# Optimization experiments

Measured on AMD Instinct MI355X. Metric: run time of the kernel, lower is better.

The kernel has to match this reference:

```python
import jax, jax.numpy as jnp
import numpy as np

N_FFT = 64
HOP = 32
PAD = N_FFT // 2

def _window():
    # torch.hann_window(n_fft) is periodic: 0.5*(1 - cos(2*pi*n/N))
    n = jnp.arange(N_FFT, dtype=jnp.float32)
    return 0.5 * (1.0 - jnp.cos(2.0 * jnp.pi * n / N_FFT))

def _frame_idx(n_frames):
    return jnp.arange(n_frames)[:, None] * HOP + jnp.arange(N_FFT)[None, :]

def _stft(x):
    # x: [..., T] -> complex spectrogram [..., n_frames, F] (torch center=True, reflect pad)
    xp = jnp.pad(x, [(0, 0)] * (x.ndim - 1) + [(PAD, PAD)], mode='reflect')
    Tp = xp.shape[-1]
    n_frames = (Tp - N_FFT) // HOP + 1
    frames = xp[..., _frame_idx(n_frames)] * _window()  # [..., n_frames, n_fft]
    return jnp.fft.rfft(frames, axis=-1)

def _istft(spec, T):
    # spec: [..., n_frames, F] -> signal [..., T] (torch istft with length=T)
    w = _window()
    frames = jnp.fft.irfft(spec, n=N_FFT, axis=-1) * w  # [..., n_frames, n_fft]
    n_frames = frames.shape[-2]
    Tp = T + 2 * PAD
    idx = _frame_idx(n_frames)
    ola = jnp.zeros(frames.shape[:-2] + (Tp,), frames.dtype).at[..., idx].add(frames)
    env = jnp.zeros((Tp,), frames.dtype).at[idx].add(w * w)
    env = jnp.where(env > 1e-11, env, 1.0)
    return (ola / env)[..., PAD:PAD + T]

def reference(x, weight):
    # x: [B, C_in, T], weight: [C_out, C_in, F]
    B, C, T = x.shape
    U = _stft(x)  # [B, C_in, n_frames, F] complex
    # Linearity: sum over input channels in frequency domain, then one ISTFT per output channel.
    Yr = jnp.einsum('oif,binf->bonf', weight, U.real)
    Yi = jnp.einsum('oif,binf->bonf', weight, U.imag)
    Y = Yr + 1j * Yi  # [B, C_out, n_frames, F]
    return _istft(Y, T)  # [B, C_out, T]

def setup_inputs() -> dict:
    key = jax.random.key(0)
    k1, k2 = jax.random.split(key)
    B, C_in, C_out, T = 8, 64, 64, 16384
    x = jax.random.normal(k1, (B, C_in, T), dtype=jnp.float32)
    weight = jax.random.normal(k2, (C_out, C_in, N_FFT // 2 + 1), dtype=jnp.float32)
    return {"x": x, "weight": weight}
```

## Files before the change

kernel.cpp:

```cpp
#include <hip/hip_runtime.h>
#include <cstddef>

#define TT 16384
#define NFRAMES 513
#define NFP 520
#define BNP (8 * NFP)
#define PI32 0.09817477042468103870f

typedef unsigned int u32;
typedef unsigned short u16;
typedef __attribute__((ext_vector_type(8))) short bf16x8;
typedef __attribute__((ext_vector_type(4))) float f32x4;

#define TAB_WBF 0
#define TAB_BM  (33 * 64 * 72)
#define TAB_BTA (TAB_BM + 80 * 72)
#define TAB_TOT (TAB_BTA + 64 * 104)
#define TF_EINV 0

__device__ __forceinline__ float b2f(u16 h) {
  union { u32 u; float f; } v; v.u = ((u32)h) << 16; return v.f;
}
__device__ __forceinline__ u16 f2b(float f) {
  union { float f; u32 u; } v; v.f = f;
  const u32 r = v.u + 0x7FFFu + ((v.u >> 16) & 1u);
  return (u16)(r >> 16);
}
__device__ __forceinline__ u32 pack2(float a, float b) {
  return (u32)f2b(a) | ((u32)f2b(b) << 16);
}
__device__ __forceinline__ float2 b2x2(u32 u) {
  union { u32 u; float f; } lo, hi;
  lo.u = u << 16; hi.u = u & 0xFFFF0000u;
  return make_float2(lo.f, hi.f);
}

__global__ __launch_bounds__(256) void k0_tables(const float* __restrict__ W,
                                                 u16* __restrict__ t16,
                                                 float* __restrict__ tf) {
  const int b = blockIdx.x, tid = threadIdx.x;
  if (b < 33) {
    for (int idx = tid; idx < 64 * 72; idx += 256) {
      const int o = idx / 72, i = idx % 72;
      const float v = (i < 64) ? W[(size_t)(o * 64 + i) * 33 + b] : 0.f;
      t16[TAB_WBF + b * 64 * 72 + idx] = f2b(v);
    }
  } else if (b == 33) {
    for (int idx = tid; idx < 80 * 72; idx += 256) {
      const int fc = idx / 72, j = idx % 72;
      float v = 0.f;
      if (j < 64 && fc < 65) {
        const float wj = 0.5f * (1.0f - cosf((float)j * PI32));
        if (fc < 64) {
          const int f = fc >> 1;
          const float ang = (float)((f * j) & 63) * PI32;
          v = wj * ((fc & 1) ? -sinf(ang) : cosf(ang));
        } else {
          v = (j & 1) ? -wj : wj;
        }
      }
      t16[TAB_BM + idx] = f2b(v);
    }
  } else {
    for (int idx = tid; idx < 64 * 104; idx += 256) {
      const int j = idx / 104, cf = idx % 104;
      float v = 0.f;
      if (cf < 66) {
        const int f = cf >> 1;
        const float wj = 0.5f * (1.0f - cosf((float)j * PI32));
        const float sc = ((f == 0) || (f == 32)) ? 0.015625f : 0.03125f;
        const float ang = (float)((f * j) & 63) * PI32;
        v = wj * sc * ((cf & 1) ? -sinf(ang) : cosf(ang));
      }
      t16[TAB_BTA + idx] = f2b(v);
    }
    if (tid < 32) {
      const float c = cosf((float)tid * PI32);
      tf[TF_EINV + tid] = 2.0f / (1.0f + c * c);
    }
  }
}

__global__ __launch_bounds__(256) void k1_stft(const float* __restrict__ x,
                                               const u16* __restrict__ t16,
                                               u16* __restrict__ U) {
  const int tile = blockIdx.x;
  const int ch   = blockIdx.y;
  const int b    = blockIdx.z;
  const int tid = threadIdx.x;
  __shared__ __align__(16) u16 Bm[80 * 72];
  __shared__ __align__(16) u16 Awt[64 * 72];
  __shared__ __align__(16) u16 Cs[66 * 72];
  __shared__ float xef[64];

  for (int k = tid; k < 720; k += 256)
    ((uint4*)Bm)[k] = ((const uint4*)(t16 + TAB_BM))[k];

  const float* xb = x + (size_t)(b * 64 + ch) * TT;

  if (tile == 8) {
    if (tid < 64) {
      const int t = (tid < 32) ? (16352 + tid) : (16414 - tid);
      xef[tid] = xb[t];
    }
    __syncthreads();
    if (tid < 66) {
      float s = 0.f;
#pragma unroll 8
      for (int j = 0; j < 64; ++j)
        s = fmaf(xef[j], b2f(Bm[tid * 72 + j]), s);
      U[(size_t)(tid * 64 + ch) * BNP + b * NFP + 512] = f2b(s);
    }
    return;
  }

  const int F0 = tile * 64;
  if (tile == 0) {
    if (tid < 32) Awt[tid] = f2b(xb[32 - tid]);
    for (int c = 8 + tid; c < 520; c += 256) {
      const float4 v = *(const float4*)(xb + 4 * c - 32);
      const uint2 pk = make_uint2(pack2(v.x, v.y), pack2(v.z, v.w));
      const int flb = c >> 3, jj = 4 * (c & 7);
      if (flb < 64) *(uint2*)&Awt[flb * 72 + jj] = pk;
      *(uint2*)&Awt[(flb - 1) * 72 + 32 + jj] = pk;
    }
  } else {
    const float* src = xb + 32 * F0 - 32;
    for (int c = tid; c < 520; c += 256) {
      const float4 v = *(const float4*)(src + 4 * c);
      const uint2 pk = make_uint2(pack2(v.x, v.y), pack2(v.z, v.w));
      const int flb = c >> 3, jj = 4 * (c & 7);
      if (flb < 64) *(uint2*)&Awt[flb * 72 + jj] = pk;
      if (flb >= 1) *(uint2*)&Awt[(flb - 1) * 72 + 32 + jj] = pk;
    }
  }
  __syncthreads();

  const int wave = tid >> 6, lane = tid & 63;
  const int n = lane & 15, quad = lane >> 4;

  bf16x8 bfr[4][2];
#pragma unroll
  for (int nt = 0; nt < 4; ++nt)
#pragma unroll
    for (int ks = 0; ks < 2; ++ks)
      bfr[nt][ks] = *(const bf16x8*)&Awt[(nt * 16 + n) * 72 + ks * 32 + quad * 8];

  const int npass = (wave == 0) ? 2 : 1;
  for (int pass = 0; pass < npass; ++pass) {
    const int mt = pass ? 4 : wave;
    bf16x8 af[2];
#pragma unroll
    for (int ks = 0; ks < 2; ++ks)
      af[ks] = *(const bf16x8*)&Bm[(mt * 16 + n) * 72 + ks * 32 + quad * 8];
    f32x4 acc[4];
#pragma unroll
    for (int nt = 0; nt < 4; ++nt) acc[nt] = (f32x4){0.f, 0.f, 0.f, 0.f};
#pragma unroll
    for (int ks = 0; ks < 2; ++ks)
#pragma unroll
      for (int nt = 0; nt < 4; ++nt)
        acc[nt] = __builtin_amdgcn_mfma_f32_16x16x32_bf16(af[ks], bfr[nt][ks],
                                                          acc[nt], 0, 0, 0);
#pragma unroll
    for (int nt = 0; nt < 4; ++nt) {
      const int fl = nt * 16 + n;
#pragma unroll
      for (int r = 0; r < 4; ++r) {
        const int fc = mt * 16 + quad * 4 + r;
        if (fc < 66) Cs[fc * 72 + fl] = f2b(acc[nt][r]);
      }
    }
  }
  __syncthreads();

  const int bnb = b * NFP + F0;
  for (int k = tid; k < 528; k += 256) {
    const int fc = k >> 3, part = k & 7;
    *(uint4*)(U + (size_t)(fc * 64 + ch) * BNP + bnb + part * 8) =
        *(const uint4*)&Cs[fc * 72 + part * 8];
  }
}

__global__ __launch_bounds__(256) void k2_mix(const u16* __restrict__ t16,
                                              u16* __restrict__ U) {
  const int f   = blockIdx.y;
  const int bn0 = blockIdx.x * 64;
  const int tid = threadIdx.x;
  __shared__ __align__(16) u16 Ut[2 * 64 * 72];
  __shared__ __align__(16) u16 Wl[64 * 72];

  for (int k = tid; k < 576; k += 256)
    ((uint4*)Wl)[k] = ((const uint4*)(t16 + TAB_WBF + f * 64 * 72))[k];

#pragma unroll
  for (int kk = 0; kk < 4; ++kk) {
    const int id = tid + kk * 256;
    const int c = id >> 9, rem = id & 511;
    const int i = rem >> 3, qc = rem & 7;
    const uint4 raw = *(const uint4*)(U + (size_t)((2 * f + c) * 64 + i) * BNP + bn0 + 8 * qc);
    const int col = (((i >> 3) ^ qc) << 3) + (i & 7);
    u16* base = &Ut[c * 4608 + col];
#pragma unroll
    for (int e = 0; e < 8; ++e) {
      const u32 w = ((const u32*)&raw)[e >> 1];
      base[(8 * qc + e) * 72] = (u16)((e & 1) ? (w >> 16) : (w & 0xFFFFu));
    }
  }
  __syncthreads();

  const int wave = tid >> 6, lane = tid & 63;
  const int n = lane & 15, quad = lane >> 4;
  const int mt = wave;

  bf16x8 af[2];
#pragma unroll
  for (int ks = 0; ks < 2; ++ks)
    af[ks] = *(const bf16x8*)&Wl[(mt * 16 + n) * 72 + ks * 32 + quad * 8];

  f32x4 acc[4][2];
#pragma unroll
  for (int nt = 0; nt < 4; ++nt)
#pragma unroll
    for (int c = 0; c < 2; ++c) acc[nt][c] = (f32x4){0.f, 0.f, 0.f, 0.f};

#pragma unroll
  for (int ks = 0; ks < 2; ++ks)
#pragma unroll
    for (int nt = 0; nt < 4; ++nt) {
      const int q = nt * 16 + n;
      const int chunk = (((ks << 2) + quad) ^ ((q >> 3) & 7)) << 3;
#pragma unroll
      for (int c = 0; c < 2; ++c) {
        const bf16x8 bf = *(const bf16x8*)&Ut[c * 4608 + q * 72 + chunk];
        acc[nt][c] = __builtin_amdgcn_mfma_f32_16x16x32_bf16(af[ks], bf,
                                                             acc[nt][c], 0, 0, 0);
      }
    }
  __syncthreads();

#pragma unroll
  for (int nt = 0; nt < 4; ++nt) {
    const int col = nt * 16 + n;
#pragma unroll
    for (int c = 0; c < 2; ++c)
#pragma unroll
      for (int r = 0; r < 4; ++r) {
        const int o = mt * 16 + quad * 4 + r;
        Ut[(c * 64 + o) * 72 + col] = f2b(acc[nt][c][r]);
      }
  }
  __syncthreads();

  for (int k = tid; k < 1024; k += 256) {
    const int row = k >> 3, part = k & 7;
    const int c = row >> 6, o = row & 63;
    *(uint4*)(U + (size_t)((2 * f + c) * 64 + o) * BNP + bn0 + part * 8) =
        *(const uint4*)&Ut[row * 72 + part * 8];
  }
}

__global__ __launch_bounds__(256) void k3_istft(const u16* __restrict__ Y,
                                                const u16* __restrict__ t16,
                                                const float* __restrict__ tf,
                                                float* __restrict__ out) {
  const int tile = blockIdx.x;
  const int o    = blockIdx.y;
  const int b    = blockIdx.z;
  const int n0 = tile * 64;
  const int tid = threadIdx.x;
  __shared__ __align__(16) u16 BtA[64 * 104];
  __shared__ __align__(16) u16 Yt[80 * 104];
  __shared__ float Csh[65 * 68];
  __shared__ float einv[32];

  for (int k = tid; k < 832; k += 256)
    ((uint4*)BtA)[k] = ((const uint4*)(t16 + TAB_BTA))[k];

  for (int id = tid; id < 1520; id += 256) {
    const int row = id / 19, c = id % 19;
    *(u32*)&Yt[row * 104 + 66 + 2 * c] = 0u;
  }
  const size_t ybase = (size_t)b * NFP + n0;
  for (int id = tid; id < 594; id += 256) {
    const int cf = id / 9, oct = id % 9;
    const uint4 raw = *(const uint4*)(Y + (size_t)(cf * 64 + o) * BNP + ybase + oct * 8);
    const u16* s = (const u16*)&raw;
#pragma unroll
    for (int e = 0; e < 8; ++e) Yt[(oct * 8 + e) * 104 + cf] = s[e];
  }
  if (tid < 32) einv[tid] = tf[TF_EINV + tid];
  __syncthreads();

  const int wave = tid >> 6, lane = tid & 63;
  const int n = lane & 15, quad = lane >> 4;
  const int mt = wave;

  bf16x8 af[3];
#pragma unroll
  for (int ks = 0; ks < 3; ++ks)
    af[ks] = *(const bf16x8*)&BtA[(mt * 16 + n) * 104 + ks * 32 + quad * 8];

  f32x4 acc[5];
#pragma unroll
  for (int nt = 0; nt < 5; ++nt) acc[nt] = (f32x4){0.f, 0.f, 0.f, 0.f};
#pragma unroll
  for (int ks = 0; ks < 3; ++ks)
#pragma unroll
    for (int nt = 0; nt < 5; ++nt) {
      const bf16x8 bf = *(const bf16x8*)&Yt[(nt * 16 + n) * 104 + ks * 32 + quad * 8];
      acc[nt] = __builtin_amdgcn_mfma_f32_16x16x32_bf16(af[ks], bf, acc[nt], 0, 0, 0);
    }
#pragma unroll
  for (int nt = 0; nt < 5; ++nt) {
    const int fl = nt * 16 + n;
    if (nt < 4 || n == 0)
      *(float4*)&Csh[fl * 68 + mt * 16 + quad * 4] =
          make_float4(acc[nt][0], acc[nt][1], acc[nt][2], acc[nt][3]);
  }
  __syncthreads();

  const int q0 = 8 * tid;
  const int j2 = q0 & 31;
  const int fl2 = 1 + (q0 >> 5);
  const float4 lo0 = *(const float4*)&Csh[fl2 * 68 + j2];
  const float4 lo1 = *(const float4*)&Csh[fl2 * 68 + j2 + 4];
  const float4 hi0 = *(const float4*)&Csh[(fl2 - 1) * 68 + j2 + 32];
  const float4 hi1 = *(const float4*)&Csh[(fl2 - 1) * 68 + j2 + 36];
  float v[8] = {lo0.x + hi0.x, lo0.y + hi0.y, lo0.z + hi0.z, lo0.w + hi0.w,
                lo1.x + hi1.x, lo1.y + hi1.y, lo1.z + hi1.z, lo1.w + hi1.w};
#pragma unroll
  for (int k = 0; k < 8; ++k) v[k] *= einv[j2 + k];
  float* po = out + (size_t)(b * 64 + o) * TT + 32 * n0 + q0;
  *(float4*)po       = make_float4(v[0], v[1], v[2], v[3]);
  *(float4*)(po + 4) = make_float4(v[4], v[5], v[6], v[7]);
}

extern "C" void kernel_launch(void* const* d_in, const int* in_sizes, int n_in,
                              void* d_out, int out_size, void* d_ws, size_t ws_size,
                              hipStream_t stream) {
  const float* x  = (const float*)d_in[0];
  const float* wt = (const float*)d_in[1];
  float* out = (float*)d_out;
  u16* U = (u16*)d_ws;
  u16* t16 = (u16*)((char*)d_ws + (size_t)66 * 64 * BNP * 2);
  float* tf = (float*)(t16 + TAB_TOT);

  dim3 blk(256);
  k0_tables<<<dim3(35),       blk, 0, stream>>>(wt, t16, tf);
  k1_stft  <<<dim3(9, 64, 8), blk, 0, stream>>>(x, t16, U);
  k2_mix   <<<dim3(65, 33),   blk, 0, stream>>>(t16, U);
  k3_istft <<<dim3(8, 64, 8), blk, 0, stream>>>(U, t16, tf, out);
}
```

Before: 149.8 us.

## Drop the table kernel and compute DFT tables inside the STFT and ISTFT blocks

Removes the separate k0_tables launch. The bf16 weight transpose moves into an extra tile column of the STFT grid, spread over 512 blocks. The windowed DFT and inverse-DFT matrices and the envelope reciprocals are now computed with sin/cos in every STFT and ISTFT block rather than loaded from a workspace table. This saves one kernel launch and a serial dependency. In exchange, every one of the thousands of blocks repeats the trig work, which adds ALU cost to both kernels.

```diff
diff --git a/kernel.cpp b/kernel.cpp
--- a/kernel.cpp
+++ b/kernel.cpp
@@ -13,10 +13,7 @@
 typedef __attribute__((ext_vector_type(4))) float f32x4;
 
 #define TAB_WBF 0
-#define TAB_BM  (33 * 64 * 72)
-#define TAB_BTA (TAB_BM + 80 * 72)
-#define TAB_TOT (TAB_BTA + 64 * 104)
-#define TF_EINV 0
+#define TAB_TOT (33 * 64 * 72)
 
 __device__ __forceinline__ float b2f(u16 h) {
   union { u32 u; float f; } v; v.u = ((u32)h) << 16; return v.f;
@@ -29,23 +26,35 @@
 __device__ __forceinline__ u32 pack2(float a, float b) {
   return (u32)f2b(a) | ((u32)f2b(b) << 16);
 }
-__device__ __forceinline__ float2 b2x2(u32 u) {
-  union { u32 u; float f; } lo, hi;
-  lo.u = u << 16; hi.u = u & 0xFFFF0000u;
-  return make_float2(lo.f, hi.f);
-}
-
-__global__ __launch_bounds__(256) void k0_tables(const float* __restrict__ W,
-                                                 u16* __restrict__ t16,
-                                                 float* __restrict__ tf) {
-  const int b = blockIdx.x, tid = threadIdx.x;
-  if (b < 33) {
-    for (int idx = tid; idx < 64 * 72; idx += 256) {
-      const int o = idx / 72, i = idx % 72;
-      const float v = (i < 64) ? W[(size_t)(o * 64 + i) * 33 + b] : 0.f;
-      t16[TAB_WBF + b * 64 * 72 + idx] = f2b(v);
-    }
-  } else if (b == 33) {
+
+__global__ __launch_bounds__(256) void k1_stft(const float* __restrict__ x,
+                                               const float* __restrict__ W,
+                                               u16* __restrict__ t16,
+                                               u16* __restrict__ U) {
+  const int tile = blockIdx.x;
+  const int ch   = blockIdx.y;
+  const int b    = blockIdx.z;
+  const int tid = threadIdx.x;
+
+  if (tile == 9) {
+    const int flat = ch * 8 + b;
+    for (int idx = flat * 256 + tid; idx < 33 * 64 * 72; idx += 512 * 256) {
+      const int f = idx / 4608, rem = idx % 4608;
+      const int o = rem / 72, i = rem % 72;
+      const float v = (i < 64) ? W[(size_t)(o * 64 + i) * 33 + f] : 0.f;
+      t16[TAB_WBF + idx] = f2b(v);
+    }
+    return;
+  }
+
+  __shared__ __align__(16) u16 Bm[80 * 72];
+  __shared__ __align__(16) u16 Awt[64 * 72];
+  __shared__ __align__(16) u16 Cs[66 * 72];
+  __shared__ float xef[64];
+
+  const float* xb = x + (size_t)(b * 64 + ch) * TT;
+
+  if (tile == 8) {
     for (int idx = tid; idx < 80 * 72; idx += 256) {
       const int fc = idx / 72, j = idx % 72;
       float v = 0.f;
@@ -59,46 +68,8 @@
           v = (j & 1) ? -wj : wj;
         }
       }
-      t16[TAB_BM + idx] = f2b(v);
-    }
-  } else {
-    for (int idx = tid; idx < 64 * 104; idx += 256) {
-      const int j = idx / 104, cf = idx % 104;
-      float v = 0.f;
-      if (cf < 66) {
-        const int f = cf >> 1;
-        const float wj = 0.5f * (1.0f - cosf((float)j * PI32));
-        const float sc = ((f == 0) || (f == 32)) ? 0.015625f : 0.03125f;
-        const float ang = (float)((f * j) & 63) * PI32;
-        v = wj * sc * ((cf & 1) ? -sinf(ang) : cosf(ang));
-      }
-      t16[TAB_BTA + idx] = f2b(v);
-    }
-    if (tid < 32) {
-      const float c = cosf((float)tid * PI32);
-      tf[TF_EINV + tid] = 2.0f / (1.0f + c * c);
-    }
-  }
-}
-
-__global__ __launch_bounds__(256) void k1_stft(const float* __restrict__ x,
-                                               const u16* __restrict__ t16,
-                                               u16* __restrict__ U) {
-  const int tile = blockIdx.x;
-  const int ch   = blockIdx.y;
-  const int b    = blockIdx.z;
-  const int tid = threadIdx.x;
-  __shared__ __align__(16) u16 Bm[80 * 72];
-  __shared__ __align__(16) u16 Awt[64 * 72];
-  __shared__ __align__(16) u16 Cs[66 * 72];
-  __shared__ float xef[64];
-
-  for (int k = tid; k < 720; k += 256)
-    ((uint4*)Bm)[k] = ((const uint4*)(t16 + TAB_BM))[k];
-
-  const float* xb = x + (size_t)(b * 64 + ch) * TT;
-
-  if (tile == 8) {
+      Bm[idx] = f2b(v);
+    }
     if (tid < 64) {
       const int t = (tid < 32) ? (16352 + tid) : (16414 - tid);
       xef[tid] = xb[t];
@@ -134,6 +105,21 @@
       if (flb >= 1) *(uint2*)&Awt[(flb - 1) * 72 + 32 + jj] = pk;
     }
   }
+  for (int idx = tid; idx < 80 * 72; idx += 256) {
+    const int fc = idx / 72, j = idx % 72;
+    float v = 0.f;
+    if (j < 64 && fc < 65) {
+      const float wj = 0.5f * (1.0f - cosf((float)j * PI32));
+      if (fc < 64) {
+        const int f = fc >> 1;
+        const float ang = (float)((f * j) & 63) * PI32;
+        v = wj * ((fc & 1) ? -sinf(ang) : cosf(ang));
+      } else {
+        v = (j & 1) ? -wj : wj;
+      }
+    }
+    Bm[idx] = f2b(v);
+  }
   __syncthreads();
 
   const int wave = tid >> 6, lane = tid & 63;
@@ -261,8 +247,6 @@
 }
 
 __global__ __launch_bounds__(256) void k3_istft(const u16* __restrict__ Y,
-                                                const u16* __restrict__ t16,
-                                                const float* __restrict__ tf,
                                                 float* __restrict__ out) {
   const int tile = blockIdx.x;
   const int o    = blockIdx.y;
@@ -274,9 +258,6 @@
   __shared__ float Csh[65 * 68];
   __shared__ float einv[32];
 
-  for (int k = tid; k < 832; k += 256)
-    ((uint4*)BtA)[k] = ((const uint4*)(t16 + TAB_BTA))[k];
-
   for (int id = tid; id < 1520; id += 256) {
     const int row = id / 19, c = id % 19;
     *(u32*)&Yt[row * 104 + 66 + 2 * c] = 0u;
@@ -289,7 +270,22 @@
 #pragma unroll
     for (int e = 0; e < 8; ++e) Yt[(oct * 8 + e) * 104 + cf] = s[e];
   }
-  if (tid < 32) einv[tid] = tf[TF_EINV + tid];
+  for (int idx = tid; idx < 64 * 104; idx += 256) {
+    const int j = idx / 104, cf = idx % 104;
+    float v = 0.f;
+    if (cf < 66) {
+      const int f = cf >> 1;
+      const float wj = 0.5f * (1.0f - cosf((float)j * PI32));
+      const float sc = ((f == 0) || (f == 32)) ? 0.015625f : 0.03125f;
+      const float ang = (float)((f * j) & 63) * PI32;
+      v = wj * sc * ((cf & 1) ? -sinf(ang) : cosf(ang));
+    }
+    BtA[idx] = f2b(v);
+  }
+  if (tid < 32) {
+    const float c = cosf((float)tid * PI32);
+    einv[tid] = 2.0f / (1.0f + c * c);
+  }
   __syncthreads();
 
   const int wave = tid >> 6, lane = tid & 63;
@@ -344,11 +340,9 @@
   float* out = (float*)d_out;
   u16* U = (u16*)d_ws;
   u16* t16 = (u16*)((char*)d_ws + (size_t)66 * 64 * BNP * 2);
-  float* tf = (float*)(t16 + TAB_TOT);
 
   dim3 blk(256);
-  k0_tables<<<dim3(35),       blk, 0, stream>>>(wt, t16, tf);
-  k1_stft  <<<dim3(9, 64, 8), blk, 0, stream>>>(x, t16, U);
-  k2_mix   <<<dim3(65, 33),   blk, 0, stream>>>(t16, U);
-  k3_istft <<<dim3(8, 64, 8), blk, 0, stream>>>(U, t16, tf, out);
-}
+  k1_stft <<<dim3(10, 64, 8), blk, 0, stream>>>(x, wt, t16, U);
+  k2_mix  <<<dim3(65, 33),    blk, 0, stream>>>(t16, U);
+  k3_istft<<<dim3(8, 64, 8),  blk, 0, stream>>>(U, out);
+}
```

Result: slower. 210.7 us (+40.7%).
